# Optimization experiments

Measured on AMD Instinct MI355X. Metric: run time of the kernel, lower is better.

Reference implementation:

```python
import math
import jax, jax.numpy as jnp
import numpy as np


def _tril_colmajor_index(d):
    # Maps packed icf tail entries (column-by-column, strictly lower) to (r, c).
    idx = np.zeros((d, d), dtype=np.int32)
    p = 0
    for c in range(d):
        for r in range(c + 1, d):
            idx[r, c] = p
            p += 1
    mask = np.tri(d, d, -1, dtype=bool)  # strictly lower triangular
    return idx, mask


def setup_inputs() -> dict:
    key = jax.random.key(0)
    k1, k2, k3, k4 = jax.random.split(key, 4)
    K, d, N = 64, 32, 50000
    icf_cols = d + d * (d - 1) // 2  # 528
    return {
        "alphas": jax.random.normal(k1, (K,), dtype=jnp.float32),
        "means": jax.random.normal(k2, (K, d), dtype=jnp.float32),
        "icf": jax.random.normal(k3, (K, icf_cols), dtype=jnp.float32),
        "x": jax.random.normal(k4, (N, d), dtype=jnp.float32),
        "wishart_gamma": jnp.ones((), dtype=jnp.float32),
        "wishart_m": jnp.ones((), dtype=jnp.float32),
    }


def reference(alphas, means, icf, x, wishart_gamma, wishart_m):
    n, d = x.shape
    k = alphas.shape[0]
    idx, mask = _tril_colmajor_index(d)
    idx = jnp.asarray(idx)
    mask = jnp.asarray(mask)

    Qdiags = jnp.exp(icf[:, :d])            # [K, d]
    sum_qs = jnp.sum(icf[:, :d], axis=1)    # [K]
    Ltail = icf[:, d:]                      # [K, d(d-1)/2]
    # Vectorized constructL: strictly-lower triangular L per component. [K, d, d]
    L = jnp.where(mask[None], Ltail[:, idx], jnp.zeros((), icf.dtype))

    xc = x[:, None, :] - means[None, :, :]  # [N, K, d]
    # Qtimesx: diag scaling + batched triangular matvec
    Lx = Qdiags[None] * xc + jnp.einsum('kij,nkj->nki', L, xc)  # [N, K, d]
    sqsum = jnp.sum(Lx * Lx, axis=2)        # [N, K]

    inner = alphas[None, :] + sum_qs[None, :] - 0.5 * sqsum
    slse = jnp.sum(jax.scipy.special.logsumexp(inner, axis=1))

    CONSTANT = -n * d * 0.5 * math.log(2 * math.pi)

    # log_wishart_prior
    nw = d + wishart_m + 1.0
    out_w = jnp.sum(0.5 * wishart_gamma * wishart_gamma
                    * (jnp.sum(Qdiags ** 2, axis=1) + jnp.sum(Ltail ** 2, axis=1))
                    - wishart_m * sum_qs)
    C = nw * d * jnp.log(wishart_gamma / math.sqrt(2.0))
    prior = out_w - k * (C - jax.scipy.special.multigammaln(0.5 * nw, d))

    return CONSTANT + slse - n * jax.scipy.special.logsumexp(alphas) + prior
```

## Files before the change

kernel.cpp:

```cpp
#include <hip/hip_runtime.h>
#include <math.h>

#define K_COMP 64
#define D 32
#define ICF_COLS 528
#define NCH 33
#define SLICES 4

typedef __attribute__((ext_vector_type(8))) short v8s;
typedef __attribute__((ext_vector_type(4))) float v4f;

__device__ __forceinline__ unsigned short f2bf(float f) {
  unsigned int u = __float_as_uint(f);
  unsigned int r = (u + 0x7FFFu + ((u >> 16) & 1u)) >> 16;
  return (unsigned short)r;
}
__device__ __forceinline__ v8s pack8(unsigned a, unsigned b, unsigned c, unsigned d) {
  union { unsigned u[4]; v8s s; } u;
  u.u[0] = a; u.u[1] = b; u.u[2] = c; u.u[3] = d; return u.s;
}
__device__ __forceinline__ v8s asv8(int4 v) {
  union { int4 i; v8s s; } u; u.i = v; return u.s;
}

__global__ __launch_bounds__(64) void gmm_prep(
    const float* __restrict__ alphas, const float* __restrict__ means,
    const float* __restrict__ icf, const float* __restrict__ wg,
    const float* __restrict__ wm,
    uint4* __restrict__ W2, float* __restrict__ eSa, float* __restrict__ wwk)
{
  int k = blockIdx.x;
  int l = threadIdx.x;
  __shared__ float M[D][D + 1];
  __shared__ float mu[D], b[D], v[D];
  __shared__ float Afl[D * D];
  __shared__ float red[64];

  const float* ick = icf + (size_t)k * ICF_COLS;

  if (l < D) {
    mu[l] = means[k * D + l];
    float q = __expf(ick[l]);
    for (int c = 0; c < D; ++c) {
      float val;
      if (c < l) { int off = c * 31 - c * (c - 1) / 2; val = ick[D + off + (l - c - 1)]; }
      else if (c == l) val = q;
      else val = 0.0f;
      M[l][c] = val;
    }
  }
  __syncthreads();
  if (l < D) {
    float acc = 0.f;
    for (int c = 0; c < D; ++c) acc = fmaf(M[l][c], mu[c], acc);
    b[l] = acc;
  }
  __syncthreads();
  if (l < D) {
    float acc = 0.f;
    for (int r = 0; r < D; ++r) acc = fmaf(M[r][l], b[r], acc);
    v[l] = acc;
  }
  for (int e = l; e < D * D; e += 64) {
    int a = e >> 5, bb = e & 31;
    float acc = 0.f;
    for (int r = 0; r < D; ++r) acc = fmaf(M[r][a], M[r][bb], acc);
    Afl[e] = -0.5f * acc;
  }
  float part = 0.f;
  for (int e = l; e < D * D; e += 64) {
    float mv = M[e / D][e % D];
    part = fmaf(mv, mv, part);
  }
  red[l] = part;
  __syncthreads();
  for (int st = 32; st > 0; st >>= 1) {
    if (l < st) red[l] += red[l + st];
    __syncthreads();
  }
  if (l == 0) {
    float msq = red[0];
    float sumq = 0.f;
    for (int i = 0; i < D; ++i) sumq += ick[i];
    float bsq = 0.f;
    for (int i = 0; i < D; ++i) bsq = fmaf(b[i], b[i], bsq);
    eSa[k] = alphas[k] + sumq - 0.5f * bsq;
    float g = wg[0], mm = wm[0];
    wwk[k] = 0.5f * g * g * msq - mm * sumq;
  }
  __syncthreads();

  int s = k >> 4, krow = k & 15;
  for (int u = l; u < NCH * 4; u += 64) {
    int c = u >> 2, g = u & 3;
    unsigned int hw[4] = {0, 0, 0, 0};
    for (int j2 = 0; j2 < 8; ++j2) {
      int bb = g * 8 + j2;
      float val = (c < D) ? Afl[c * 32 + bb] : v[bb];
      hw[j2 >> 1] |= ((unsigned int)f2bf(val)) << (16 * (j2 & 1));
    }
    W2[(s * NCH + c) * 64 + g * 16 + krow] = make_uint4(hw[0], hw[1], hw[2], hw[3]);
  }
}

__global__ __launch_bounds__(256, 4) void gmm_main(
    const float* __restrict__ x, const int4* __restrict__ W2,
    const float* __restrict__ eSa, int N, float* __restrict__ partials)
{
  int tid = threadIdx.x;
  int lane = tid & 63;
  int wv = tid >> 6;
  int w = blockIdx.x * 4 + wv;
  int n16 = lane & 15, g = lane >> 4;

  int pt0 = (2 * w) * 16 + n16;
  int pt1 = (2 * w + 1) * 16 + n16;
  bool pv0 = pt0 < N, pv1 = pt1 < N;
  const float* xr0 = x + (size_t)(pv0 ? pt0 : (N - 1)) * D;
  const float* xr1 = x + (size_t)(pv1 ? pt1 : (N - 1)) * D;

  int bb = g * 8;
  float xb0[8], xb1[8];
  {
    float4 a0 = *reinterpret_cast<const float4*>(xr0 + bb);
    float4 a1 = *reinterpret_cast<const float4*>(xr0 + bb + 4);
    float4 c0 = *reinterpret_cast<const float4*>(xr1 + bb);
    float4 c1 = *reinterpret_cast<const float4*>(xr1 + bb + 4);
    xb0[0]=a0.x; xb0[1]=a0.y; xb0[2]=a0.z; xb0[3]=a0.w;
    xb0[4]=a1.x; xb0[5]=a1.y; xb0[6]=a1.z; xb0[7]=a1.w;
    xb1[0]=c0.x; xb1[1]=c0.y; xb1[2]=c0.z; xb1[3]=c0.w;
    xb1[4]=c1.x; xb1[5]=c1.y; xb1[6]=c1.z; xb1[7]=c1.w;
  }

  const int4* wp = W2 + lane;
  v4f acc[2][SLICES];
#pragma unroll
  for (int t = 0; t < 2; ++t)
#pragma unroll
    for (int s = 0; s < SLICES; ++s) acc[t][s] = (v4f){0.f, 0.f, 0.f, 0.f};

  int4 Ac[SLICES], An[SLICES];
#pragma unroll
  for (int s = 0; s < SLICES; ++s) Ac[s] = wp[(s * NCH) * 64];

#pragma unroll 1
  for (int c = 0; c < NCH; ++c) {
    if (c + 1 < NCH) {
#pragma unroll
      for (int s = 0; s < SLICES; ++s) An[s] = wp[(s * NCH + c + 1) * 64];
    }
    float xa0 = 1.0f, xa1 = 1.0f;
    if (c < D) { xa0 = xr0[c]; xa1 = xr1[c]; }

    unsigned d0[4], d1[4];
#pragma unroll
    for (int q = 0; q < 4; ++q) {
      d0[q] = (unsigned)f2bf(xa0 * xb0[2*q]) | ((unsigned)f2bf(xa0 * xb0[2*q+1]) << 16);
      d1[q] = (unsigned)f2bf(xa1 * xb1[2*q]) | ((unsigned)f2bf(xa1 * xb1[2*q+1]) << 16);
    }
    v8s B0 = pack8(d0[0], d0[1], d0[2], d0[3]);
    v8s B1 = pack8(d1[0], d1[1], d1[2], d1[3]);

#pragma unroll
    for (int s = 0; s < SLICES; ++s) {
      v8s As = asv8(Ac[s]);
      acc[0][s] = __builtin_amdgcn_mfma_f32_16x16x32_bf16(As, B0, acc[0][s], 0, 0, 0);
      acc[1][s] = __builtin_amdgcn_mfma_f32_16x16x32_bf16(As, B1, acc[1][s], 0, 0, 0);
    }
#pragma unroll
    for (int s = 0; s < SLICES; ++s) Ac[s] = An[s];
  }

  const float4* esp = reinterpret_cast<const float4*>(eSa);
  float tsum[2];
#pragma unroll
  for (int t = 0; t < 2; ++t) {
    float vals[16];
#pragma unroll
    for (int s = 0; s < SLICES; ++s) {
      float4 es = esp[s * 4 + g];
      vals[s*4+0] = acc[t][s].x + es.x;
      vals[s*4+1] = acc[t][s].y + es.y;
      vals[s*4+2] = acc[t][s].z + es.z;
      vals[s*4+3] = acc[t][s].w + es.w;
    }
    float m = vals[0];
#pragma unroll
    for (int i = 1; i < 16; ++i) m = fmaxf(m, vals[i]);
    float sv = 0.f;
#pragma unroll
    for (int i = 0; i < 16; ++i) sv += __expf(vals[i] - m);
#pragma unroll
    for (int off = 16; off <= 32; off <<= 1) {
      float mo = __shfl_xor(m, off);
      float so = __shfl_xor(sv, off);
      float mn = fmaxf(m, mo);
      sv = sv * __expf(m - mn) + so * __expf(mo - mn);
      m = mn;
    }
    bool pv = (t == 0) ? pv0 : pv1;
    float lse = pv ? (m + __logf(sv)) : 0.f;
#pragma unroll
    for (int off = 8; off > 0; off >>= 1) lse += __shfl_down(lse, off);
    tsum[t] = lse;
  }
  if (lane == 0) partials[w] = tsum[0] + tsum[1];
}

__global__ __launch_bounds__(256) void gmm_final(
    const float* __restrict__ wwk, const float* __restrict__ partials, int nparts,
    const float* __restrict__ alphas, const float* __restrict__ wg,
    const float* __restrict__ wm, int N, float* __restrict__ out)
{
  int tid = threadIdx.x;
  __shared__ double sd[256];
  __shared__ float samax;
  __shared__ double s_slse, s_sa, s_ow;

  double acc = 0.0;
  for (int i = tid; i < nparts; i += 256) acc += (double)partials[i];
  sd[tid] = acc;
  __syncthreads();
  for (int st = 128; st > 0; st >>= 1) {
    if (tid < st) sd[tid] += sd[tid + st];
    __syncthreads();
  }
  if (tid == 0) s_slse = sd[0];
  __syncthreads();

  if (tid < 64) {
    float m = alphas[tid];
#pragma unroll
    for (int off = 32; off > 0; off >>= 1) m = fmaxf(m, __shfl_xor(m, off));
    if (tid == 0) samax = m;
  }
  __syncthreads();

  sd[tid] = (tid < K_COMP) ? exp((double)(alphas[tid] - samax)) : 0.0;
  __syncthreads();
  for (int st = 128; st > 0; st >>= 1) {
    if (tid < st) sd[tid] += sd[tid + st];
    __syncthreads();
  }
  if (tid == 0) s_sa = sd[0];
  __syncthreads();

  sd[tid] = (tid < K_COMP) ? (double)wwk[tid] : 0.0;
  __syncthreads();
  for (int st = 128; st > 0; st >>= 1) {
    if (tid < st) sd[tid] += sd[tid + st];
    __syncthreads();
  }
  if (tid == 0) s_ow = sd[0];
  __syncthreads();

  double nw = (double)D + (double)wm[0] + 1.0;
  sd[tid] = (tid < D) ? lgamma(0.5 * nw + (1.0 - (double)(tid + 1)) * 0.5) : 0.0;
  __syncthreads();
  for (int st = 128; st > 0; st >>= 1) {
    if (tid < st) sd[tid] += sd[tid + st];
    __syncthreads();
  }

  if (tid == 0) {
    double mg = (D * (D - 1) / 4.0) * log(M_PI) + sd[0];
    double lse_a = (double)samax + log(s_sa);
    double g = (double)wg[0];
    double C = nw * (double)D * log(g / sqrt(2.0));
    double CONST = -(double)N * D * 0.5 * log(2.0 * M_PI);
    double prior = s_ow - (double)K_COMP * (C - mg);
    out[0] = (float)(CONST + s_slse - (double)N * lse_a + prior);
  }
}

extern "C" void kernel_launch(void* const* d_in, const int* in_sizes, int n_in,
                              void* d_out, int out_size, void* d_ws, size_t ws_size,
                              hipStream_t stream)
{
  const float* alphas = (const float*)d_in[0];
  const float* means  = (const float*)d_in[1];
  const float* icf    = (const float*)d_in[2];
  const float* x      = (const float*)d_in[3];
  const float* wg     = (const float*)d_in[4];
  const float* wm     = (const float*)d_in[5];
  float* out = (float*)d_out;

  int N = in_sizes[3] / D;
  int ntiles = (N + 15) / 16;
  int nwaves = (ntiles + 1) / 2;
  int nblk   = (nwaves + 3) / 4;
  int nparts = nblk * 4;

  char* wsb = (char*)d_ws;
  const size_t W2BYTES = (size_t)SLICES * NCH * 64 * 16;
  uint4* W2  = (uint4*)wsb;
  float* eSa = (float*)(wsb + W2BYTES);
  float* wwk = eSa + K_COMP;
  float* partials = wwk + K_COMP;

  gmm_prep<<<K_COMP, 64, 0, stream>>>(alphas, means, icf, wg, wm, W2, eSa, wwk);
  gmm_main<<<nblk, 256, 0, stream>>>(x, (const int4*)W2, eSa, N, partials);
  gmm_final<<<1, 256, 0, stream>>>(wwk, partials, nparts, alphas, wg, wm, N, out);
}
```

Before: 48.95 us.

## Give each wave one 16-point tile and simplify final-kernel lgamma reduction

The main kernel now handles one 16-point tile per wave instead of two, which doubles the wave count and drops the explicit A-fragment double-buffering in favour of a fully unrolled chunk loop. Each wave still loads all of W2, so W2 traffic per point doubles, but register pressure falls and more waves are available to hide latency. The final kernel replaces per-dimension lgamma calls with two lgamma values plus log terms derived from the recurrence, and swaps the double exp for __expf. This lowers serial cost in the single-block epilogue at a small cost in precision.

```diff
diff --git a/kernel.cpp b/kernel.cpp
--- a/kernel.cpp
+++ b/kernel.cpp
@@ -6,6 +6,7 @@
 #define ICF_COLS 528
 #define NCH 33
 #define SLICES 4
+#define PTSW 16
 
 typedef __attribute__((ext_vector_type(8))) short v8s;
 typedef __attribute__((ext_vector_type(4))) float v4f;
@@ -103,7 +104,7 @@
   }
 }
 
-__global__ __launch_bounds__(256, 4) void gmm_main(
+__global__ __launch_bounds__(256) void gmm_main(
     const float* __restrict__ x, const int4* __restrict__ W2,
     const float* __restrict__ eSa, int N, float* __restrict__ partials)
 {
@@ -113,98 +114,64 @@
   int w = blockIdx.x * 4 + wv;
   int n16 = lane & 15, g = lane >> 4;
 
-  int pt0 = (2 * w) * 16 + n16;
-  int pt1 = (2 * w + 1) * 16 + n16;
-  bool pv0 = pt0 < N, pv1 = pt1 < N;
-  const float* xr0 = x + (size_t)(pv0 ? pt0 : (N - 1)) * D;
-  const float* xr1 = x + (size_t)(pv1 ? pt1 : (N - 1)) * D;
-
-  int bb = g * 8;
-  float xb0[8], xb1[8];
+  int pt = w * PTSW + n16;
+  bool pv = pt < N;
+  const float* xr = x + (size_t)(pv ? pt : (N - 1)) * D;
+
+  float xb[8];
   {
-    float4 a0 = *reinterpret_cast<const float4*>(xr0 + bb);
-    float4 a1 = *reinterpret_cast<const float4*>(xr0 + bb + 4);
-    float4 c0 = *reinterpret_cast<const float4*>(xr1 + bb);
-    float4 c1 = *reinterpret_cast<const float4*>(xr1 + bb + 4);
-    xb0[0]=a0.x; xb0[1]=a0.y; xb0[2]=a0.z; xb0[3]=a0.w;
-    xb0[4]=a1.x; xb0[5]=a1.y; xb0[6]=a1.z; xb0[7]=a1.w;
-    xb1[0]=c0.x; xb1[1]=c0.y; xb1[2]=c0.z; xb1[3]=c0.w;
-    xb1[4]=c1.x; xb1[5]=c1.y; xb1[6]=c1.z; xb1[7]=c1.w;
+    float4 a0 = *reinterpret_cast<const float4*>(xr + g * 8);
+    float4 a1 = *reinterpret_cast<const float4*>(xr + g * 8 + 4);
+    xb[0] = a0.x; xb[1] = a0.y; xb[2] = a0.z; xb[3] = a0.w;
+    xb[4] = a1.x; xb[5] = a1.y; xb[6] = a1.z; xb[7] = a1.w;
   }
 
   const int4* wp = W2 + lane;
-  v4f acc[2][SLICES];
-#pragma unroll
-  for (int t = 0; t < 2; ++t)
-#pragma unroll
-    for (int s = 0; s < SLICES; ++s) acc[t][s] = (v4f){0.f, 0.f, 0.f, 0.f};
-
-  int4 Ac[SLICES], An[SLICES];
-#pragma unroll
-  for (int s = 0; s < SLICES; ++s) Ac[s] = wp[(s * NCH) * 64];
-
-#pragma unroll 1
+  v4f acc[SLICES];
+#pragma unroll
+  for (int s = 0; s < SLICES; ++s) acc[s] = (v4f){0.f, 0.f, 0.f, 0.f};
+
+#pragma unroll
   for (int c = 0; c < NCH; ++c) {
-    if (c + 1 < NCH) {
-#pragma unroll
-      for (int s = 0; s < SLICES; ++s) An[s] = wp[(s * NCH + c + 1) * 64];
-    }
-    float xa0 = 1.0f, xa1 = 1.0f;
-    if (c < D) { xa0 = xr0[c]; xa1 = xr1[c]; }
-
-    unsigned d0[4], d1[4];
-#pragma unroll
-    for (int q = 0; q < 4; ++q) {
-      d0[q] = (unsigned)f2bf(xa0 * xb0[2*q]) | ((unsigned)f2bf(xa0 * xb0[2*q+1]) << 16);
-      d1[q] = (unsigned)f2bf(xa1 * xb1[2*q]) | ((unsigned)f2bf(xa1 * xb1[2*q+1]) << 16);
-    }
-    v8s B0 = pack8(d0[0], d0[1], d0[2], d0[3]);
-    v8s B1 = pack8(d1[0], d1[1], d1[2], d1[3]);
-
-#pragma unroll
-    for (int s = 0; s < SLICES; ++s) {
-      v8s As = asv8(Ac[s]);
-      acc[0][s] = __builtin_amdgcn_mfma_f32_16x16x32_bf16(As, B0, acc[0][s], 0, 0, 0);
-      acc[1][s] = __builtin_amdgcn_mfma_f32_16x16x32_bf16(As, B1, acc[1][s], 0, 0, 0);
-    }
-#pragma unroll
-    for (int s = 0; s < SLICES; ++s) Ac[s] = An[s];
+    float xa = (c < D) ? xr[c] : 1.0f;
+    unsigned d0 = (unsigned)f2bf(xa * xb[0]) | ((unsigned)f2bf(xa * xb[1]) << 16);
+    unsigned d1 = (unsigned)f2bf(xa * xb[2]) | ((unsigned)f2bf(xa * xb[3]) << 16);
+    unsigned d2 = (unsigned)f2bf(xa * xb[4]) | ((unsigned)f2bf(xa * xb[5]) << 16);
+    unsigned d3 = (unsigned)f2bf(xa * xb[6]) | ((unsigned)f2bf(xa * xb[7]) << 16);
+    v8s B = pack8(d0, d1, d2, d3);
+#pragma unroll
+    for (int s = 0; s < SLICES; ++s)
+      acc[s] = __builtin_amdgcn_mfma_f32_16x16x32_bf16(asv8(wp[(s * NCH + c) * 64]), B, acc[s], 0, 0, 0);
   }
 
   const float4* esp = reinterpret_cast<const float4*>(eSa);
-  float tsum[2];
-#pragma unroll
-  for (int t = 0; t < 2; ++t) {
-    float vals[16];
-#pragma unroll
-    for (int s = 0; s < SLICES; ++s) {
-      float4 es = esp[s * 4 + g];
-      vals[s*4+0] = acc[t][s].x + es.x;
-      vals[s*4+1] = acc[t][s].y + es.y;
-      vals[s*4+2] = acc[t][s].z + es.z;
-      vals[s*4+3] = acc[t][s].w + es.w;
-    }
-    float m = vals[0];
-#pragma unroll
-    for (int i = 1; i < 16; ++i) m = fmaxf(m, vals[i]);
-    float sv = 0.f;
-#pragma unroll
-    for (int i = 0; i < 16; ++i) sv += __expf(vals[i] - m);
-#pragma unroll
-    for (int off = 16; off <= 32; off <<= 1) {
-      float mo = __shfl_xor(m, off);
-      float so = __shfl_xor(sv, off);
-      float mn = fmaxf(m, mo);
-      sv = sv * __expf(m - mn) + so * __expf(mo - mn);
-      m = mn;
-    }
-    bool pv = (t == 0) ? pv0 : pv1;
-    float lse = pv ? (m + __logf(sv)) : 0.f;
-#pragma unroll
-    for (int off = 8; off > 0; off >>= 1) lse += __shfl_down(lse, off);
-    tsum[t] = lse;
-  }
-  if (lane == 0) partials[w] = tsum[0] + tsum[1];
+  float vals[16];
+#pragma unroll
+  for (int s = 0; s < SLICES; ++s) {
+    float4 es = esp[s * 4 + g];
+    vals[s * 4 + 0] = acc[s].x + es.x;
+    vals[s * 4 + 1] = acc[s].y + es.y;
+    vals[s * 4 + 2] = acc[s].z + es.z;
+    vals[s * 4 + 3] = acc[s].w + es.w;
+  }
+  float m = vals[0];
+#pragma unroll
+  for (int i = 1; i < 16; ++i) m = fmaxf(m, vals[i]);
+  float sv = 0.f;
+#pragma unroll
+  for (int i = 0; i < 16; ++i) sv += __expf(vals[i] - m);
+#pragma unroll
+  for (int off = 16; off <= 32; off <<= 1) {
+    float mo = __shfl_xor(m, off);
+    float so = __shfl_xor(sv, off);
+    float mn = fmaxf(m, mo);
+    sv = sv * __expf(m - mn) + so * __expf(mo - mn);
+    m = mn;
+  }
+  float lse = pv ? (m + __logf(sv)) : 0.f;
+#pragma unroll
+  for (int off = 8; off > 0; off >>= 1) lse += __shfl_down(lse, off);
+  if (lane == 0) partials[w] = lse;
 }
 
 __global__ __launch_bounds__(256) void gmm_final(
@@ -236,7 +203,7 @@
   }
   __syncthreads();
 
-  sd[tid] = (tid < K_COMP) ? exp((double)(alphas[tid] - samax)) : 0.0;
+  sd[tid] = (tid < K_COMP) ? (double)__expf(alphas[tid] - samax) : 0.0;
   __syncthreads();
   for (int st = 128; st > 0; st >>= 1) {
     if (tid < st) sd[tid] += sd[tid + st];
@@ -255,7 +222,14 @@
   __syncthreads();
 
   double nw = (double)D + (double)wm[0] + 1.0;
-  sd[tid] = (tid < D) ? lgamma(0.5 * nw + (1.0 - (double)(tid + 1)) * 0.5) : 0.0;
+  double a  = 0.5 * nw;
+  double bh = a - 0.5;
+  double contrib = 0.0;
+  if (tid == 0)      contrib = 16.0 * lgamma(a);
+  else if (tid == 1) contrib = 16.0 * lgamma(bh);
+  else if (tid >= 2 && tid < 17)  { int k = tid - 1;  contrib = -(double)(16 - k) * log(a  - (double)k); }
+  else if (tid >= 17 && tid < 32) { int k = tid - 16; contrib = -(double)(16 - k) * log(bh - (double)k); }
+  sd[tid] = contrib;
   __syncthreads();
   for (int st = 128; st > 0; st >>= 1) {
     if (tid < st) sd[tid] += sd[tid + st];
@@ -286,8 +260,7 @@
   float* out = (float*)d_out;
 
   int N = in_sizes[3] / D;
-  int ntiles = (N + 15) / 16;
-  int nwaves = (ntiles + 1) / 2;
+  int nwaves = (N + PTSW - 1) / PTSW;
   int nblk   = (nwaves + 3) / 4;
   int nparts = nblk * 4;
 
```

New measurement: 47.36 us. 3.2% less time.
